# Kernel optimization log

Measured on AMD Instinct MI355X. Metric: run time of the kernel, lower is better.

Reference implementation:

```python
import jax, jax.numpy as jnp
import numpy as np

N_EL, N_NB, DIM = 8192, 24, 256
CUTOFF = 5.0
F0, F1 = 32, 16
N_ENV = 8
N_FEAT = 4  # [dist, dx, dy, dz]


def setup_inputs() -> dict:
    key = jax.random.key(0)
    ks = jax.random.split(key, 24)
    d = {}
    d['elec'] = jax.random.normal(ks[0], (N_EL, DIM), jnp.float32)
    d['msg'] = jax.random.normal(ks[1], (N_EL, DIM), jnp.float32)
    # positions inside a box of half the cutoff so pairs are within range
    d['r'] = jax.random.uniform(ks[2], (N_EL, 3), jnp.float32) * (0.5 * CUTOFF)
    d['r_nb'] = jax.random.uniform(ks[3], (N_EL, N_NB, 3), jnp.float32) * (0.5 * CUTOFF)
    d['s'] = jax.random.randint(ks[4], (N_EL,), 0, 2, jnp.int32)
    d['s_nb'] = jax.random.randint(ks[5], (N_EL, N_NB), 0, 2, jnp.int32)
    d['hinit_nb'] = jax.random.normal(ks[6], (N_EL, N_NB, DIM), jnp.float32)
    # parameters
    def lecun(k, shape):
        fan_in = shape[0]
        return jax.random.normal(k, shape, jnp.float32) / np.float32(np.sqrt(fan_in))
    d['W_in'] = lecun(ks[7], (DIM, DIM)); d['b_in'] = jnp.zeros((DIM,), jnp.float32)
    d['ee_scales'] = jax.random.uniform(ks[8], (N_ENV,), jnp.float32, 0.5, CUTOFF)
    d['ee_kernel'] = lecun(ks[9], (N_FEAT, F0))
    d['ee_bias'] = 2.0 * jax.random.normal(ks[10], (F0,), jnp.float32)
    d['Wf'] = lecun(ks[11], (F0 + N_ENV, F1)); d['bf'] = jnp.zeros((F1,), jnp.float32)
    d['Wsame'] = lecun(ks[12], (F1, DIM))
    d['Wdiff'] = lecun(ks[13], (F1, DIM))
    d['W1'] = lecun(ks[14], (DIM, DIM)); d['b1'] = jnp.zeros((DIM,), jnp.float32)
    d['W2'] = lecun(ks[15], (DIM, DIM)); d['b2'] = jnp.zeros((DIM,), jnp.float32)
    d['W3'] = lecun(ks[16], (DIM, DIM)); d['b3'] = jnp.zeros((DIM,), jnp.float32)
    d['scale'] = jnp.float32(1.0)  # FixedScalingFactor (identity at init)
    return d


def _forward(elec, msg, r, r_nb, s, s_nb, hinit_nb,
             W_in, b_in, ee_scales, ee_kernel, ee_bias, Wf, bf,
             Wsame, Wdiff, W1, b1, W2, b2, W3, b3, scale):
    silu = jax.nn.silu
    elec1 = silu(elec @ W_in + b_in)                       # [N, D]
    # get_diff_features: [dist, dx, dy, dz]
    diff = r_nb - r[:, None, :]                             # [N, K, 3]
    dist = jnp.sqrt(jnp.sum(diff * diff, -1) + 1e-12)       # [N, K]
    feats = jnp.concatenate([dist[..., None], diff], -1)    # [N, K, 4]
    spin_mask = s[:, None] == s_nb                          # [N, K]
    # PairwiseFilter: MLP on diff-features + radial envelopes, smooth cutoff
    env = jnp.exp(-jnp.square(dist[..., None] / ee_scales)) # [N, K, E]
    h = silu(feats @ ee_kernel + ee_bias)                   # [N, K, F0]
    h = jnp.concatenate([h, env], -1)                       # [N, K, F0+E]
    x = dist / CUTOFF
    cut = jnp.where(dist < CUTOFF, jnp.square(1.0 - x) * (1.0 + 2.0 * x), 0.0)
    beta = (h @ Wf + bf) * cut[..., None]                   # [N, K, F1]
    gamma = jnp.where(spin_mask[..., None], beta @ Wsame, beta @ Wdiff)  # [N, K, D]
    hinit_msg = jnp.einsum('nid,nid->nd', silu(elec1[:, None] + hinit_nb), gamma)
    out = silu(elec1 @ W1 + b1 + hinit_msg)
    out = silu(out @ W2 + b2 + msg)
    out = silu(out @ W3 + b3)
    return (out + elec1) * scale


def reference(elec, msg, r, r_nb, s, s_nb, hinit_nb,
              W_in, b_in, ee_scales, ee_kernel, ee_bias, Wf, bf,
              Wsame, Wdiff, W1, b1, W2, b2, W3, b3, scale):
    return _forward(elec, msg, r, r_nb, s, s_nb, hinit_nb,
                    W_in, b_in, ee_scales, ee_kernel, ee_bias, Wf, bf,
                    Wsame, Wdiff, W1, b1, W2, b2, W3, b3, scale)
```

## Files before the change

kernel.cpp:

```cpp
#include <hip/hip_runtime.h>

#define DIM 256
#define PDIM 260
#define NNB 24
#define NEL 8192
#define ROWS 16
#define NT 512
#define CUTOFF 5.0f

typedef unsigned int u32;
typedef unsigned short u16;
typedef __attribute__((ext_vector_type(8))) short bf16x8;
typedef __attribute__((ext_vector_type(4))) float f32x4;

__device__ __forceinline__ u16 f2b(float f){
  union{float f;u32 i;}v; v.f=f;
  u32 r = v.i + 0x7fffu + ((v.i>>16)&1u);
  return (u16)(r>>16);
}
__device__ __forceinline__ float fast_silu(float x){
  float e = __builtin_amdgcn_exp2f(-1.44269504088896340f * x);
  return x * __builtin_amdgcn_rcpf(1.0f + e);
}

__global__ __launch_bounds__(256)
void wprep(const float* __restrict__ W0, const float* __restrict__ W1,
           const float* __restrict__ W2, const float* __restrict__ W3,
           u16* __restrict__ ws){
  const int mat = blockIdx.x >> 8;
  const int n   = blockIdx.x & 255;
  const int k   = threadIdx.x;
  const float* W = (mat==0)?W0:(mat==1)?W1:(mat==2)?W2:W3;
  ws[(mat<<16) + (n<<8) + k] = f2b(W[(k<<8) + n]);
}

template<int MODE>
__device__ __forceinline__ void gemm_mfma(
    const float* A, float* sE1, float* sR1,
    const u16* __restrict__ Wt, const float* __restrict__ bias,
    const float* __restrict__ extraGbl, float* __restrict__ outGbl,
    float scl, int n0, int t)
{
  const int lane = t & 63;
  const int ln   = lane & 15;
  const int quad = lane >> 4;
  const int nt0  = (t >> 6) << 1;
  f32x4 acc0 = {0.f,0.f,0.f,0.f};
  f32x4 acc1 = {0.f,0.f,0.f,0.f};
  const float* arow = A + ln*PDIM;
  const u16* bp0 = Wt + (nt0*16 + ln)*DIM;
  const u16* bp1 = bp0 + 16*DIM;
  #pragma unroll
  for (int ks = 0; ks < 8; ks++){
    const int k0 = ks*32 + quad*8;
    float4 a01 = *(const float4*)(arow + k0);
    float4 a23 = *(const float4*)(arow + k0 + 4);
    bf16x8 af;
    af[0]=(short)f2b(a01.x); af[1]=(short)f2b(a01.y);
    af[2]=(short)f2b(a01.z); af[3]=(short)f2b(a01.w);
    af[4]=(short)f2b(a23.x); af[5]=(short)f2b(a23.y);
    af[6]=(short)f2b(a23.z); af[7]=(short)f2b(a23.w);
    bf16x8 b0 = *(const bf16x8*)(bp0 + k0);
    bf16x8 b1 = *(const bf16x8*)(bp1 + k0);
    acc0 = __builtin_amdgcn_mfma_f32_16x16x32_bf16(af, b0, acc0, 0, 0, 0);
    acc1 = __builtin_amdgcn_mfma_f32_16x16x32_bf16(af, b1, acc1, 0, 0, 0);
  }
  if (MODE == 2) __syncthreads();
  #pragma unroll
  for (int r = 0; r < 4; r++){
    const int m = quad*4 + r;
    #pragma unroll
    for (int tt = 0; tt < 2; tt++){
      const int n = (nt0+tt)*16 + ln;
      float v = (tt ? acc1[r] : acc0[r]) + bias[n];
      if (MODE == 1) v += sR1[m*PDIM + n];
      if (MODE == 2) v += extraGbl[(size_t)(n0+m)*DIM + n];
      v = fast_silu(v);
      if (MODE == 0)      sE1[m*PDIM + n] = v;
      else if (MODE == 3) outGbl[(size_t)(n0+m)*DIM + n] = (v + sE1[m*PDIM + n]) * scl;
      else                sR1[m*PDIM + n] = v;
    }
  }
}

__global__ __launch_bounds__(NT, 4)
void fused_moon_kernel(
    const float* __restrict__ elec, const float* __restrict__ msg,
    const float* __restrict__ rpos, const float* __restrict__ rnb,
    const int* __restrict__ s,    const int* __restrict__ snb,
    const float* __restrict__ hinit,
    const float* __restrict__ bin,
    const float* __restrict__ eesc, const float* __restrict__ eek,
    const float* __restrict__ eeb,  const float* __restrict__ Wf,
    const float* __restrict__ bfb,  const float* __restrict__ Wsame,
    const float* __restrict__ Wdiff,
    const float* __restrict__ b1, const float* __restrict__ b2,
    const float* __restrict__ b3,
    const float* __restrict__ scalep,
    const u16* __restrict__ Wt,
    float* __restrict__ out)
{
  __shared__ float sR1[ROWS*PDIM];
  __shared__ float sB [ROWS*NNB*16];
  __shared__ float sE1[ROWS*PDIM];
  __shared__ int   sMask[ROWS*NNB];

  const int t  = threadIdx.x;
  const int n0 = blockIdx.x * ROWS;

  {
    const float4* ep = (const float4*)elec;
    #pragma unroll
    for (int h = 0; h < 2; h++){
      const int idx = t + h*NT;
      float4 v = ep[(size_t)n0*64 + idx];
      *(float4*)&sR1[(idx>>6)*PDIM + (idx&63)*4] = v;
    }
  }
  __syncthreads();

  gemm_mfma<0>(sR1, sE1, sR1, Wt, bin, nullptr, nullptr, 0.f, n0, t);

  if (t < ROWS*NNB) {
    const int rr = t / NNB;
    const int k  = t - rr*NNB;
    const int n  = n0 + rr;
    const float* rp  = rpos + n*3;
    const float* rnp = rnb + (n*NNB + k)*3;
    float dx = rnp[0] - rp[0];
    float dy = rnp[1] - rp[1];
    float dz = rnp[2] - rp[2];
    float dist = sqrtf(dx*dx + dy*dy + dz*dz + 1e-12f);
    float feats[4] = {dist, dx, dy, dz};
    float h[32];
    #pragma unroll
    for (int f4 = 0; f4 < 8; f4++){
      float4 a4 = *(const float4*)&eeb[4*f4];
      float av[4] = {a4.x, a4.y, a4.z, a4.w};
      #pragma unroll
      for (int i = 0; i < 4; i++){
        float4 kv = *(const float4*)&eek[i*32 + 4*f4];
        av[0]+=feats[i]*kv.x; av[1]+=feats[i]*kv.y; av[2]+=feats[i]*kv.z; av[3]+=feats[i]*kv.w;
      }
      h[4*f4+0]=fast_silu(av[0]); h[4*f4+1]=fast_silu(av[1]);
      h[4*f4+2]=fast_silu(av[2]); h[4*f4+3]=fast_silu(av[3]);
    }
    float env[8];
    #pragma unroll
    for (int e = 0; e < 8; e++){
      float q = dist * __builtin_amdgcn_rcpf(eesc[e]);
      env[e] = __builtin_amdgcn_exp2f(-1.44269504088896340f * q * q);
    }
    float xx = dist * (1.0f/CUTOFF);
    float cut = (dist < CUTOFF) ? (1.0f-xx)*(1.0f-xx)*(1.0f+2.0f*xx) : 0.0f;
    float* bout = &sB[(rr*NNB + k)*16];
    #pragma unroll
    for (int j4 = 0; j4 < 4; j4++){
      float4 a4 = *(const float4*)&bfb[4*j4];
      float av[4] = {a4.x, a4.y, a4.z, a4.w};
      #pragma unroll
      for (int f = 0; f < 40; f++){
        float val = (f < 32) ? h[f] : env[f-32];
        float4 wv = *(const float4*)&Wf[f*16 + 4*j4];
        av[0]+=val*wv.x; av[1]+=val*wv.y; av[2]+=val*wv.z; av[3]+=val*wv.w;
      }
      *(float4*)(bout + 4*j4) = make_float4(av[0]*cut, av[1]*cut, av[2]*cut, av[3]*cut);
    }
    sMask[rr*NNB + k] = (s[n] == snb[n*NNB + k]) ? 1 : 0;
  }
  __syncthreads();

  {
    const int rg = t >> 7;
    const int d0 = (t & 127) << 1;
    float2 wsv[16], wdv[16];
    #pragma unroll
    for (int j = 0; j < 16; j++){
      wsv[j] = *(const float2*)(Wsame + j*DIM + d0);
      wdv[j] = *(const float2*)(Wdiff + j*DIM + d0);
    }
    for (int rr = 0; rr < 4; rr++){
      const int r = rg*4 + rr;
      const int n = n0 + r;
      float2 e1v = *(const float2*)&sE1[r*PDIM + d0];
      float ax = 0.f, ay = 0.f;
      for (int k = 0; k < NNB; k++){
        const float* bp = &sB[(r*NNB + k)*16];
        float bb[16];
        *(float4*)&bb[0]  = *(const float4*)(bp);
        *(float4*)&bb[4]  = *(const float4*)(bp+4);
        *(float4*)&bb[8]  = *(const float4*)(bp+8);
        *(float4*)&bb[12] = *(const float4*)(bp+12);
        float2 hv = *(const float2*)(hinit + ((size_t)(n*NNB + k) << 8) + d0);
        float sx = fast_silu(e1v.x + hv.x);
        float sy = fast_silu(e1v.y + hv.y);
        float gx = 0.f, gy = 0.f;
        if (sMask[r*NNB + k]){
          #pragma unroll
          for (int j = 0; j < 16; j++){ gx += bb[j]*wsv[j].x; gy += bb[j]*wsv[j].y; }
        } else {
          #pragma unroll
          for (int j = 0; j < 16; j++){ gx += bb[j]*wdv[j].x; gy += bb[j]*wdv[j].y; }
        }
        ax += sx*gx; ay += sy*gy;
      }
      *(float2*)&sR1[r*PDIM + d0] = make_float2(ax, ay);
    }
  }
  __syncthreads();

  const float scl = scalep[0];

  gemm_mfma<1>(sE1, sE1, sR1, Wt + (1<<16), b1, nullptr, nullptr, 0.f, n0, t);
  __syncthreads();
  gemm_mfma<2>(sR1, sE1, sR1, Wt + (2<<16), b2, msg, nullptr, 0.f, n0, t);
  __syncthreads();
  gemm_mfma<3>(sR1, sE1, sR1, Wt + (3<<16), b3, nullptr, out, scl, n0, t);
}

extern "C" void kernel_launch(void* const* d_in, const int* in_sizes, int n_in,
                              void* d_out, int out_size, void* d_ws, size_t ws_size,
                              hipStream_t stream) {
  (void)in_sizes; (void)n_in; (void)ws_size; (void)out_size;
  const float* elec  = (const float*)d_in[0];
  const float* msg   = (const float*)d_in[1];
  const float* rpos  = (const float*)d_in[2];
  const float* rnb   = (const float*)d_in[3];
  const int*   s     = (const int*)d_in[4];
  const int*   snb   = (const int*)d_in[5];
  const float* hinit = (const float*)d_in[6];
  const float* Win   = (const float*)d_in[7];
  const float* bin   = (const float*)d_in[8];
  const float* eesc  = (const float*)d_in[9];
  const float* eek   = (const float*)d_in[10];
  const float* eeb   = (const float*)d_in[11];
  const float* Wf    = (const float*)d_in[12];
  const float* bfb   = (const float*)d_in[13];
  const float* Wsame = (const float*)d_in[14];
  const float* Wdiff = (const float*)d_in[15];
  const float* W1    = (const float*)d_in[16];
  const float* b1    = (const float*)d_in[17];
  const float* W2    = (const float*)d_in[18];
  const float* b2    = (const float*)d_in[19];
  const float* W3    = (const float*)d_in[20];
  const float* b3    = (const float*)d_in[21];
  const float* scl   = (const float*)d_in[22];
  float* outp        = (float*)d_out;
  u16*   wt          = (u16*)d_ws;

  wprep<<<dim3(1024), dim3(256), 0, stream>>>(Win, W1, W2, W3, wt);
  fused_moon_kernel<<<dim3(NEL/ROWS), dim3(NT), 0, stream>>>(
      elec, msg, rpos, rnb, s, snb, hinit,
      bin, eesc, eek, eeb, Wf, bfb, Wsame, Wdiff,
      b1, b2, b3, scl, wt, outp);
}
```

Before: 392.0 us.

## Compute pairwise gamma via MFMA with masked concatenated Wsame/Wdiff and bf16 elec1

Replaces the scalar per-neighbour gamma computation (16-term dot products selecting Wsame or Wdiff by spin mask) with a bf16 MFMA. Beta is written into a zero-padded, swizzled 32-wide shared tile whose halves are masked by spin, and multiplied against a pre-converted concatenated [Wsame;Wdiff] weight. elec1 is now kept in shared memory as bf16 to shrink LDS usage, and the occupancy hint is raised from 4 to 6. The hinit read pattern moves to the MFMA output layout, 16 lanes wide per row. This adds bf16 rounding to beta, gamma and elec1, which changes numerics including the final residual add.

```diff
diff --git a/kernel.cpp b/kernel.cpp
--- a/kernel.cpp
+++ b/kernel.cpp
@@ -2,6 +2,7 @@
 
 #define DIM 256
 #define PDIM 260
+#define PD2  264
 #define NNB 24
 #define NEL 8192
 #define ROWS 16
@@ -18,6 +19,9 @@
   u32 r = v.i + 0x7fffu + ((v.i>>16)&1u);
   return (u16)(r>>16);
 }
+__device__ __forceinline__ float b2f(u16 u){
+  union{u32 i;float f;}v; v.i = ((u32)u)<<16; return v.f;
+}
 __device__ __forceinline__ float fast_silu(float x){
   float e = __builtin_amdgcn_exp2f(-1.44269504088896340f * x);
   return x * __builtin_amdgcn_rcpf(1.0f + e);
@@ -26,17 +30,28 @@
 __global__ __launch_bounds__(256)
 void wprep(const float* __restrict__ W0, const float* __restrict__ W1,
            const float* __restrict__ W2, const float* __restrict__ W3,
+           const float* __restrict__ Wsame, const float* __restrict__ Wdiff,
            u16* __restrict__ ws){
-  const int mat = blockIdx.x >> 8;
-  const int n   = blockIdx.x & 255;
-  const int k   = threadIdx.x;
-  const float* W = (mat==0)?W0:(mat==1)?W1:(mat==2)?W2:W3;
-  ws[(mat<<16) + (n<<8) + k] = f2b(W[(k<<8) + n]);
-}
-
-template<int MODE>
+  if (blockIdx.x < 1024){
+    const int mat = blockIdx.x >> 8;
+    const int n   = blockIdx.x & 255;
+    const int k   = threadIdx.x;
+    const float* W = (mat==0)?W0:(mat==1)?W1:(mat==2)?W2:W3;
+    ws[(mat<<16) + (n<<8) + k] = f2b(W[(k<<8) + n]);
+  } else {
+    const int n = threadIdx.x;
+    u16* dst = ws + 4*65536 + n*32;
+    #pragma unroll
+    for (int kk = 0; kk < 16; kk++){
+      dst[kk]    = f2b(Wsame[kk*DIM + n]);
+      dst[16+kk] = f2b(Wdiff[kk*DIM + n]);
+    }
+  }
+}
+
+template<int MODE, int ABF16>
 __device__ __forceinline__ void gemm_mfma(
-    const float* A, float* sE1, float* sR1,
+    const void* A, u16* sE1b, float* sR1,
     const u16* __restrict__ Wt, const float* __restrict__ bias,
     const float* __restrict__ extraGbl, float* __restrict__ outGbl,
     float scl, int n0, int t)
@@ -47,19 +62,23 @@
   const int nt0  = (t >> 6) << 1;
   f32x4 acc0 = {0.f,0.f,0.f,0.f};
   f32x4 acc1 = {0.f,0.f,0.f,0.f};
-  const float* arow = A + ln*PDIM;
   const u16* bp0 = Wt + (nt0*16 + ln)*DIM;
   const u16* bp1 = bp0 + 16*DIM;
   #pragma unroll
   for (int ks = 0; ks < 8; ks++){
     const int k0 = ks*32 + quad*8;
-    float4 a01 = *(const float4*)(arow + k0);
-    float4 a23 = *(const float4*)(arow + k0 + 4);
     bf16x8 af;
-    af[0]=(short)f2b(a01.x); af[1]=(short)f2b(a01.y);
-    af[2]=(short)f2b(a01.z); af[3]=(short)f2b(a01.w);
-    af[4]=(short)f2b(a23.x); af[5]=(short)f2b(a23.y);
-    af[6]=(short)f2b(a23.z); af[7]=(short)f2b(a23.w);
+    if (ABF16){
+      af = *(const bf16x8*)((const u16*)A + ln*PD2 + k0);
+    } else {
+      const float* arow = (const float*)A + ln*PDIM;
+      float4 a01 = *(const float4*)(arow + k0);
+      float4 a23 = *(const float4*)(arow + k0 + 4);
+      af[0]=(short)f2b(a01.x); af[1]=(short)f2b(a01.y);
+      af[2]=(short)f2b(a01.z); af[3]=(short)f2b(a01.w);
+      af[4]=(short)f2b(a23.x); af[5]=(short)f2b(a23.y);
+      af[6]=(short)f2b(a23.z); af[7]=(short)f2b(a23.w);
+    }
     bf16x8 b0 = *(const bf16x8*)(bp0 + k0);
     bf16x8 b1 = *(const bf16x8*)(bp1 + k0);
     acc0 = __builtin_amdgcn_mfma_f32_16x16x32_bf16(af, b0, acc0, 0, 0, 0);
@@ -76,14 +95,14 @@
       if (MODE == 1) v += sR1[m*PDIM + n];
       if (MODE == 2) v += extraGbl[(size_t)(n0+m)*DIM + n];
       v = fast_silu(v);
-      if (MODE == 0)      sE1[m*PDIM + n] = v;
-      else if (MODE == 3) outGbl[(size_t)(n0+m)*DIM + n] = (v + sE1[m*PDIM + n]) * scl;
+      if (MODE == 0)      sE1b[m*PD2 + n] = f2b(v);
+      else if (MODE == 3) outGbl[(size_t)(n0+m)*DIM + n] = (v + b2f(sE1b[m*PD2 + n])) * scl;
       else                sR1[m*PDIM + n] = v;
     }
   }
 }
 
-__global__ __launch_bounds__(NT, 4)
+__global__ __launch_bounds__(NT, 6)
 void fused_moon_kernel(
     const float* __restrict__ elec, const float* __restrict__ msg,
     const float* __restrict__ rpos, const float* __restrict__ rnb,
@@ -92,8 +111,7 @@
     const float* __restrict__ bin,
     const float* __restrict__ eesc, const float* __restrict__ eek,
     const float* __restrict__ eeb,  const float* __restrict__ Wf,
-    const float* __restrict__ bfb,  const float* __restrict__ Wsame,
-    const float* __restrict__ Wdiff,
+    const float* __restrict__ bfb,
     const float* __restrict__ b1, const float* __restrict__ b2,
     const float* __restrict__ b3,
     const float* __restrict__ scalep,
@@ -101,10 +119,8 @@
     float* __restrict__ out)
 {
   __shared__ float sR1[ROWS*PDIM];
-  __shared__ float sB [ROWS*NNB*16];
-  __shared__ float sE1[ROWS*PDIM];
-  __shared__ int   sMask[ROWS*NNB];
-
+  __shared__ u16   sE1b[ROWS*PD2];
+  __shared__ u16   sBC[NNB*16*32];
   const int t  = threadIdx.x;
   const int n0 = blockIdx.x * ROWS;
 
@@ -119,7 +135,7 @@
   }
   __syncthreads();
 
-  gemm_mfma<0>(sR1, sE1, sR1, Wt, bin, nullptr, nullptr, 0.f, n0, t);
+  gemm_mfma<0,0>(sR1, sE1b, sR1, Wt, bin, nullptr, nullptr, 0.f, n0, t);
 
   if (t < ROWS*NNB) {
     const int rr = t / NNB;
@@ -153,7 +169,7 @@
     }
     float xx = dist * (1.0f/CUTOFF);
     float cut = (dist < CUTOFF) ? (1.0f-xx)*(1.0f-xx)*(1.0f+2.0f*xx) : 0.0f;
-    float* bout = &sB[(rr*NNB + k)*16];
+    float barr[16];
     #pragma unroll
     for (int j4 = 0; j4 < 4; j4++){
       float4 a4 = *(const float4*)&bfb[4*j4];
@@ -164,58 +180,77 @@
         float4 wv = *(const float4*)&Wf[f*16 + 4*j4];
         av[0]+=val*wv.x; av[1]+=val*wv.y; av[2]+=val*wv.z; av[3]+=val*wv.w;
       }
-      *(float4*)(bout + 4*j4) = make_float4(av[0]*cut, av[1]*cut, av[2]*cut, av[3]*cut);
-    }
-    sMask[rr*NNB + k] = (s[n] == snb[n*NNB + k]) ? 1 : 0;
+      barr[4*j4+0]=av[0]*cut; barr[4*j4+1]=av[1]*cut;
+      barr[4*j4+2]=av[2]*cut; barr[4*j4+3]=av[3]*cut;
+    }
+    const int m = (s[n] == snb[n*NNB + k]);
+    u16 vals[32];
+    #pragma unroll
+    for (int j = 0; j < 16; j++){
+      u16 b = f2b(barr[j]);
+      vals[j]    = m ? b : (u16)0;
+      vals[16+j] = m ? (u16)0 : b;
+    }
+    u16* rowp = &sBC[(k*16 + rr)*32];
+    #pragma unroll
+    for (int c = 0; c < 4; c++){
+      const int cp = c ^ ((rr>>1)&3);
+      bf16x8 cv;
+      #pragma unroll
+      for (int j = 0; j < 8; j++) cv[j] = (short)vals[c*8 + j];
+      *(bf16x8*)(rowp + cp*8) = cv;
+    }
   }
   __syncthreads();
 
   {
-    const int rg = t >> 7;
-    const int d0 = (t & 127) << 1;
-    float2 wsv[16], wdv[16];
-    #pragma unroll
-    for (int j = 0; j < 16; j++){
-      wsv[j] = *(const float2*)(Wsame + j*DIM + d0);
-      wdv[j] = *(const float2*)(Wdiff + j*DIM + d0);
-    }
-    for (int rr = 0; rr < 4; rr++){
-      const int r = rg*4 + rr;
-      const int n = n0 + r;
-      float2 e1v = *(const float2*)&sE1[r*PDIM + d0];
-      float ax = 0.f, ay = 0.f;
-      for (int k = 0; k < NNB; k++){
-        const float* bp = &sB[(r*NNB + k)*16];
-        float bb[16];
-        *(float4*)&bb[0]  = *(const float4*)(bp);
-        *(float4*)&bb[4]  = *(const float4*)(bp+4);
-        *(float4*)&bb[8]  = *(const float4*)(bp+8);
-        *(float4*)&bb[12] = *(const float4*)(bp+12);
-        float2 hv = *(const float2*)(hinit + ((size_t)(n*NNB + k) << 8) + d0);
-        float sx = fast_silu(e1v.x + hv.x);
-        float sy = fast_silu(e1v.y + hv.y);
-        float gx = 0.f, gy = 0.f;
-        if (sMask[r*NNB + k]){
-          #pragma unroll
-          for (int j = 0; j < 16; j++){ gx += bb[j]*wsv[j].x; gy += bb[j]*wsv[j].y; }
-        } else {
-          #pragma unroll
-          for (int j = 0; j < 16; j++){ gx += bb[j]*wdv[j].x; gy += bb[j]*wdv[j].y; }
-        }
-        ax += sx*gx; ay += sy*gy;
-      }
-      *(float2*)&sR1[r*PDIM + d0] = make_float2(ax, ay);
+    const int lane = t & 63;
+    const int ln   = lane & 15;
+    const int quad = lane >> 4;
+    const int nt0  = (t >> 6) << 1;
+    const u16* Wcat = Wt + 4*65536;
+    bf16x8 bs0 = *(const bf16x8*)(Wcat + (nt0*16 + ln)*32 + quad*8);
+    bf16x8 bs1 = *(const bf16x8*)(Wcat + ((nt0+1)*16 + ln)*32 + quad*8);
+    float e1v[4][2], hm[4][2];
+    #pragma unroll
+    for (int j = 0; j < 4; j++){
+      #pragma unroll
+      for (int tt = 0; tt < 2; tt++){
+        e1v[j][tt] = b2f(sE1b[(quad*4+j)*PD2 + (nt0+tt)*16 + ln]);
+        hm[j][tt] = 0.f;
+      }
+    }
+    const int cswz = (quad ^ ((ln>>1)&3))*8;
+    const float* hb = hinit + (size_t)(n0 + quad*4)*NNB*DIM + ln;
+    for (int k = 0; k < NNB; k++){
+      bf16x8 af = *(const bf16x8*)(&sBC[(k*16 + ln)*32 + cswz]);
+      f32x4 z = {0.f,0.f,0.f,0.f};
+      f32x4 g0 = __builtin_amdgcn_mfma_f32_16x16x32_bf16(af, bs0, z, 0, 0, 0);
+      f32x4 g1 = __builtin_amdgcn_mfma_f32_16x16x32_bf16(af, bs1, z, 0, 0, 0);
+      #pragma unroll
+      for (int j = 0; j < 4; j++){
+        const float* hp = hb + ((size_t)(j*NNB + k))*DIM + nt0*16;
+        float h0 = hp[0];
+        float h1 = hp[16];
+        hm[j][0] += fast_silu(e1v[j][0] + h0) * g0[j];
+        hm[j][1] += fast_silu(e1v[j][1] + h1) * g1[j];
+      }
+    }
+    #pragma unroll
+    for (int j = 0; j < 4; j++){
+      sR1[(quad*4+j)*PDIM + nt0*16 + ln]     = hm[j][0];
+      sR1[(quad*4+j)*PDIM + (nt0+1)*16 + ln] = hm[j][1];
     }
   }
   __syncthreads();
 
   const float scl = scalep[0];
 
-  gemm_mfma<1>(sE1, sE1, sR1, Wt + (1<<16), b1, nullptr, nullptr, 0.f, n0, t);
-  __syncthreads();
-  gemm_mfma<2>(sR1, sE1, sR1, Wt + (2<<16), b2, msg, nullptr, 0.f, n0, t);
-  __syncthreads();
-  gemm_mfma<3>(sR1, sE1, sR1, Wt + (3<<16), b3, nullptr, out, scl, n0, t);
+  gemm_mfma<1,1>(sE1b, sE1b, sR1, Wt + (1<<16), b1, nullptr, nullptr, 0.f, n0, t);
+  __syncthreads();
+  gemm_mfma<2,0>(sR1, sE1b, sR1, Wt + (2<<16), b2, msg, nullptr, 0.f, n0, t);
+  __syncthreads();
+  gemm_mfma<3,0>(sR1, sE1b, sR1, Wt + (3<<16), b3, nullptr, out, scl, n0, t);
 }
 
 extern "C" void kernel_launch(void* const* d_in, const int* in_sizes, int n_in,
@@ -248,9 +283,9 @@
   float* outp        = (float*)d_out;
   u16*   wt          = (u16*)d_ws;
 
-  wprep<<<dim3(1024), dim3(256), 0, stream>>>(Win, W1, W2, W3, wt);
+  wprep<<<dim3(1025), dim3(256), 0, stream>>>(Win, W1, W2, W3, Wsame, Wdiff, wt);
   fused_moon_kernel<<<dim3(NEL/ROWS), dim3(NT), 0, stream>>>(
       elec, msg, rpos, rnb, s, snb, hinit,
-      bin, eesc, eek, eeb, Wf, bfb, Wsame, Wdiff,
+      bin, eesc, eek, eeb, Wf, bfb,
       b1, b2, b3, scl, wt, outp);
 }
```

New measurement: 419.9 us. +7.1%, slower.
